# Kernel tuning notes

Measured on AMD Instinct MI355X. Metric: run time of the kernel, lower is better.

Reference implementation:

```python
import jax, jax.numpy as jnp
import numpy as np

SPARSITY = 0.9  # target fraction of zeros (magnitude pruning)
D_IN = 4096
D_OUT = 4096
TOKENS = 4096


def setup_inputs() -> dict:
    key = jax.random.key(0)
    k1, k2 = jax.random.split(key)
    x = jax.random.normal(k1, (TOKENS, D_IN), dtype=jnp.float32)
    weight = jax.random.normal(k2, (D_OUT, D_IN), dtype=jnp.float32) * 0.01
    bias = jnp.zeros((D_OUT,), dtype=jnp.float32)
    return {"x": x, "weight": weight, "bias": bias}


def reference(x, weight, bias):
    # Magnitude pruning: threshold at the SPARSITY quantile of |W|,
    # keep only entries strictly above threshold (matches CSR build),
    # then sparse-dense GEMM y = x @ W_pruned^T + b.
    aw = jnp.abs(weight)
    thr = jnp.quantile(aw, SPARSITY)
    w_pruned = jnp.where(aw > thr, weight, jnp.zeros_like(weight))
    return x @ w_pruned.T + bias
```

## Files before the change

kernel.cpp:

```cpp
#include <hip/hip_runtime.h>
#include <stdint.h>

#define D_IN   4096
#define D_OUT  4096
#define NTOK   4096
#define NW     (D_OUT * D_IN)
#define RANK1  15099493u

typedef unsigned int  uint32;
typedef unsigned short ushort_t;
typedef float  f32x4  __attribute__((ext_vector_type(4)));
typedef __bf16 bf16x8 __attribute__((ext_vector_type(8)));

__device__ __forceinline__ uint32 rne_bf16(float f) {
  uint32 u = __float_as_uint(f);
  return (u + 0x7FFFu + ((u >> 16) & 1u)) >> 16;
}

__device__ __forceinline__ void gload_lds16(const void* g, void* l) {
  __builtin_amdgcn_global_load_lds((__attribute__((address_space(1))) void*)(g),
                                   (__attribute__((address_space(3))) void*)(l), 16, 0, 0);
}

template <int NB>
__device__ __forceinline__ void dsel(const uint32* __restrict__ h, uint32 rank,
                                     uint32* res, uint32* wtot) {
  constexpr int PER = NB >> 8;
  int tid = threadIdx.x;
  int lane = tid & 63, wid = tid >> 6;
  uint32 loc[PER];
  uint32 s = 0;
  int base = tid * PER;
#pragma unroll
  for (int i = 0; i < PER; i++) { loc[i] = h[base + i]; s += loc[i]; }
  uint32 v = s;
  for (int d = 1; d < 64; d <<= 1) { uint32 o = __shfl_up(v, (unsigned)d); if (lane >= d) v += o; }
  if (lane == 63) wtot[wid] = v;
  __syncthreads();
  uint32 woff = 0;
  for (int w = 0; w < wid; w++) woff += wtot[w];
  uint32 incl = v + woff, excl = incl - s;
  if (rank >= excl && rank < incl) {
    uint32 c = excl;
#pragma unroll
    for (int i = 0; i < PER; i++) {
      if (rank < c + loc[i]) { res[0] = (uint32)(base + i); res[1] = rank - c; break; }
      c += loc[i];
    }
  }
  __syncthreads();
}

__global__ void k1_hist1_convx(const uint4* __restrict__ wb, uint32* __restrict__ hist,
                               const float4* __restrict__ x, uint4* __restrict__ xout) {
  __shared__ uint32 lh[4][2048];
  if (blockIdx.x < 2048) {
    for (int i = threadIdx.x; i < 8192; i += 256) ((uint32*)lh)[i] = 0;
    __syncthreads();
    int wid = threadIdx.x >> 6;
    int idx = blockIdx.x * 256 + threadIdx.x;
    for (int i = idx; i < NW / 4; i += 2048 * 256) {
      uint4 v = wb[i];
      atomicAdd(&lh[wid][(v.x & 0x7FFFFFFFu) >> 20], 1u);
      atomicAdd(&lh[wid][(v.y & 0x7FFFFFFFu) >> 20], 1u);
      atomicAdd(&lh[wid][(v.z & 0x7FFFFFFFu) >> 20], 1u);
      atomicAdd(&lh[wid][(v.w & 0x7FFFFFFFu) >> 20], 1u);
    }
    __syncthreads();
    for (int i = threadIdx.x; i < 2048; i += 256) {
      uint32 c = lh[0][i] + lh[1][i] + lh[2][i] + lh[3][i];
      if (c) atomicAdd(&hist[i], c);
    }
  } else {
    int i = (blockIdx.x - 2048) * 256 + threadIdx.x;
    for (; i < NW / 8; i += 1024 * 256) {
      float4 a = x[2 * i], b = x[2 * i + 1];
      uint4 o;
      o.x = rne_bf16(a.x) | (rne_bf16(a.y) << 16);
      o.y = rne_bf16(a.z) | (rne_bf16(a.w) << 16);
      o.z = rne_bf16(b.x) | (rne_bf16(b.y) << 16);
      o.w = rne_bf16(b.z) | (rne_bf16(b.w) << 16);
      xout[i] = o;
    }
  }
}

__global__ void k2_hist2(const uint4* __restrict__ wb, const uint32* __restrict__ hist1,
                         uint32* __restrict__ hist2) {
  __shared__ uint32 lh[1024];
  __shared__ uint32 res1[2], wt[4];
  for (int i = threadIdx.x; i < 1024; i += 256) lh[i] = 0;
  dsel<2048>(hist1, RANK1, res1, wt);
  uint32 pref = res1[0];
  int idx = blockIdx.x * 256 + threadIdx.x;
  for (int i = idx; i < NW / 4; i += 2048 * 256) {
    uint4 v = wb[i];
    uint32 k;
    k = v.x & 0x7FFFFFFFu; if ((k >> 20) == pref) atomicAdd(&lh[(k >> 10) & 1023u], 1u);
    k = v.y & 0x7FFFFFFFu; if ((k >> 20) == pref) atomicAdd(&lh[(k >> 10) & 1023u], 1u);
    k = v.z & 0x7FFFFFFFu; if ((k >> 20) == pref) atomicAdd(&lh[(k >> 10) & 1023u], 1u);
    k = v.w & 0x7FFFFFFFu; if ((k >> 20) == pref) atomicAdd(&lh[(k >> 10) & 1023u], 1u);
  }
  __syncthreads();
  for (int i = threadIdx.x; i < 1024; i += 256) { uint32 c = lh[i]; if (c) atomicAdd(&hist2[i], c); }
}

__global__ void k3_hist3(const uint4* __restrict__ wb, const uint32* __restrict__ hist1,
                         const uint32* __restrict__ hist2, uint32* __restrict__ hist3) {
  __shared__ uint32 lh[1024];
  __shared__ uint32 res1[2], res2[2], wt[4];
  for (int i = threadIdx.x; i < 1024; i += 256) lh[i] = 0;
  dsel<2048>(hist1, RANK1, res1, wt);
  dsel<1024>(hist2, res1[1], res2, wt);
  uint32 pref = (res1[0] << 10) | res2[0];
  int idx = blockIdx.x * 256 + threadIdx.x;
  for (int i = idx; i < NW / 4; i += 2048 * 256) {
    uint4 v = wb[i];
    uint32 k;
    k = v.x & 0x7FFFFFFFu; if ((k >> 10) == pref) atomicAdd(&lh[k & 1023u], 1u);
    k = v.y & 0x7FFFFFFFu; if ((k >> 10) == pref) atomicAdd(&lh[k & 1023u], 1u);
    k = v.z & 0x7FFFFFFFu; if ((k >> 10) == pref) atomicAdd(&lh[k & 1023u], 1u);
    k = v.w & 0x7FFFFFFFu; if ((k >> 10) == pref) atomicAdd(&lh[k & 1023u], 1u);
  }
  __syncthreads();
  for (int i = threadIdx.x; i < 1024; i += 256) { uint32 c = lh[i]; if (c) atomicAdd(&hist3[i], c); }
}

__global__ void k4_convw(const float4* __restrict__ w, const uint32* __restrict__ hist1,
                         const uint32* __restrict__ hist2, const uint32* __restrict__ hist3,
                         uint4* __restrict__ out) {
  __shared__ uint32 res1[2], res2[2], res3[2], wt[4];
  dsel<2048>(hist1, RANK1, res1, wt);
  dsel<1024>(hist2, res1[1], res2, wt);
  dsel<1024>(hist3, res2[1], res3, wt);
  float thr = __uint_as_float((res1[0] << 20) | (res2[0] << 10) | res3[0]);
  int i = blockIdx.x * 256 + threadIdx.x;
  for (; i < NW / 8; i += 2048 * 256) {
    float4 a = w[2 * i], b = w[2 * i + 1];
    float f[8] = {a.x, a.y, a.z, a.w, b.x, b.y, b.z, b.w};
    uint32 h[8];
#pragma unroll
    for (int j = 0; j < 8; j++) h[j] = (fabsf(f[j]) > thr) ? rne_bf16(f[j]) : 0u;
    uint4 o;
    o.x = h[0] | (h[1] << 16);
    o.y = h[2] | (h[3] << 16);
    o.z = h[4] | (h[5] << 16);
    o.w = h[6] | (h[7] << 16);
    out[i] = o;
  }
}

#define TILES 128

__global__ __launch_bounds__(512, 2) void gemm_bt(const ushort_t* __restrict__ A,
                                                  const ushort_t* __restrict__ B,
                                                  const float* __restrict__ bias,
                                                  float* __restrict__ C) {
  extern __shared__ ushort_t lds[];

  int bid = blockIdx.x;
  int swz = (bid & 7) * 32 + (bid >> 3);
  int bm = swz >> 4;
  int bn = swz & 15;

  int tid  = threadIdx.x;
  int lane = tid & 63;
  int wave = tid >> 6;
  int wm = wave >> 2, wn = wave & 3;

  int l15  = lane & 15;
  int csel = (lane >> 4) ^ ((lane >> 1) & 3);

  int idx0 = tid, idx1 = 512 + tid;
  int sr0 = idx0 >> 2, scl0 = (idx0 & 3) ^ ((sr0 >> 1) & 3);
  int sr1 = idx1 >> 2, scl1 = (idx1 & 3) ^ ((sr1 >> 1) & 3);
  int ld0 = idx0 * 8, ld1 = idx1 * 8;
  const ushort_t* pA0 = A + (size_t)(bm * 256 + sr0) * D_IN + scl0 * 8;
  const ushort_t* pA1 = A + (size_t)(bm * 256 + sr1) * D_IN + scl1 * 8;
  const ushort_t* pB0 = B + (size_t)(bn * 256 + sr0) * D_IN + scl0 * 8;
  const ushort_t* pB1 = B + (size_t)(bn * 256 + sr1) * D_IN + scl1 * 8;

  f32x4 acc[8][4];
#pragma unroll
  for (int m = 0; m < 8; m++)
#pragma unroll
    for (int n = 0; n < 4; n++) acc[m][n] = (f32x4){0.f, 0.f, 0.f, 0.f};

  gload_lds16(pA0,      lds + ld0);         gload_lds16(pA1,      lds + ld1);
  gload_lds16(pB0,      lds + 8192 + ld0);  gload_lds16(pB1,      lds + 8192 + ld1);
  gload_lds16(pA0 + 32, lds + 16384 + ld0); gload_lds16(pA1 + 32, lds + 16384 + ld1);
  gload_lds16(pB0 + 32, lds + 24576 + ld0); gload_lds16(pB1 + 32, lds + 24576 + ld1);
  pA0 += 64; pA1 += 64; pB0 += 64; pB1 += 64;
  asm volatile("s_waitcnt vmcnt(4)" ::: "memory");
  asm volatile("s_barrier" ::: "memory");

  int ar = wm * 128 + l15;
  int br = wn * 64 + l15;

  int cur = 0, sd = 2;
  for (int t = 0; t < TILES; t++) {
    ushort_t* sbase = lds + sd * 16384;
    const bf16x8* A8 = (const bf16x8*)(lds + cur * 16384);
    const bf16x8* B8 = A8 + 1024;

    bf16x8 bv0, bv1, bv2, bv3, a0, a1, a2, a3, a4, a5, a6, a7;
    bv0 = B8[(br +  0) * 4 + csel];
    bv1 = B8[(br + 16) * 4 + csel];
    bv2 = B8[(br + 32) * 4 + csel];
    bv3 = B8[(br + 48) * 4 + csel];
    a0  = A8[(ar +  0) * 4 + csel];
    a1  = A8[(ar + 16) * 4 + csel];
    __builtin_amdgcn_sched_barrier(0);
    a2  = A8[(ar + 32) * 4 + csel];
    a3  = A8[(ar + 48) * 4 + csel];
    a4  = A8[(ar + 64) * 4 + csel];
    a5  = A8[(ar + 80) * 4 + csel];
    a6  = A8[(ar + 96) * 4 + csel];
    a7  = A8[(ar + 112) * 4 + csel];
    __builtin_amdgcn_sched_barrier(0);
    gload_lds16(pA0, sbase + ld0);
    gload_lds16(pA1, sbase + ld1);
    gload_lds16(pB0, sbase + 8192 + ld0);
    gload_lds16(pB1, sbase + 8192 + ld1);
    __builtin_amdgcn_sched_barrier(0);

    asm volatile("s_waitcnt lgkmcnt(6)" ::: "memory");
    __builtin_amdgcn_sched_barrier(0);
    __builtin_amdgcn_s_setprio(1);
#pragma unroll
    for (int n = 0; n < 4; n++) {
      bf16x8 bvv = (n == 0) ? bv0 : (n == 1) ? bv1 : (n == 2) ? bv2 : bv3;
      acc[0][n] = __builtin_amdgcn_mfma_f32_16x16x32_bf16(a0, bvv, acc[0][n], 0, 0, 0);
      acc[1][n] = __builtin_amdgcn_mfma_f32_16x16x32_bf16(a1, bvv, acc[1][n], 0, 0, 0);
    }
    __builtin_amdgcn_s_setprio(0);

    asm volatile("s_waitcnt lgkmcnt(4)" ::: "memory");
    __builtin_amdgcn_sched_barrier(0);
    __builtin_amdgcn_s_setprio(1);
#pragma unroll
    for (int n = 0; n < 4; n++) {
      bf16x8 bvv = (n == 0) ? bv0 : (n == 1) ? bv1 : (n == 2) ? bv2 : bv3;
      acc[2][n] = __builtin_amdgcn_mfma_f32_16x16x32_bf16(a2, bvv, acc[2][n], 0, 0, 0);
      acc[3][n] = __builtin_amdgcn_mfma_f32_16x16x32_bf16(a3, bvv, acc[3][n], 0, 0, 0);
    }
    __builtin_amdgcn_s_setprio(0);

    asm volatile("s_waitcnt lgkmcnt(2)" ::: "memory");
    __builtin_amdgcn_sched_barrier(0);
    __builtin_amdgcn_s_setprio(1);
#pragma unroll
    for (int n = 0; n < 4; n++) {
      bf16x8 bvv = (n == 0) ? bv0 : (n == 1) ? bv1 : (n == 2) ? bv2 : bv3;
      acc[4][n] = __builtin_amdgcn_mfma_f32_16x16x32_bf16(a4, bvv, acc[4][n], 0, 0, 0);
      acc[5][n] = __builtin_amdgcn_mfma_f32_16x16x32_bf16(a5, bvv, acc[5][n], 0, 0, 0);
    }
    __builtin_amdgcn_s_setprio(0);

    asm volatile("s_waitcnt vmcnt(4) lgkmcnt(0)" ::: "memory");
    asm volatile("s_barrier" ::: "memory");
    __builtin_amdgcn_sched_barrier(0);
    __builtin_amdgcn_s_setprio(1);
#pragma unroll
    for (int n = 0; n < 4; n++) {
      bf16x8 bvv = (n == 0) ? bv0 : (n == 1) ? bv1 : (n == 2) ? bv2 : bv3;
      acc[6][n] = __builtin_amdgcn_mfma_f32_16x16x32_bf16(a6, bvv, acc[6][n], 0, 0, 0);
      acc[7][n] = __builtin_amdgcn_mfma_f32_16x16x32_bf16(a7, bvv, acc[7][n], 0, 0, 0);
    }
    __builtin_amdgcn_s_setprio(0);

    if (t < TILES - 3) { pA0 += 32; pA1 += 32; pB0 += 32; pB1 += 32; }
    cur = (cur == 2) ? 0 : cur + 1;
    sd  = (sd  == 2) ? 0 : sd + 1;
  }

  int orow0 = bm * 256 + wm * 128 + (lane >> 4) * 4;
  int ocol0 = bn * 256 + wn * 64 + l15;
#pragma unroll
  for (int n = 0; n < 4; n++) {
    float bv2 = bias[ocol0 + n * 16];
#pragma unroll
    for (int m = 0; m < 8; m++) {
#pragma unroll
      for (int r = 0; r < 4; r++) {
        C[(size_t)(orow0 + m * 16 + r) * D_OUT + ocol0 + n * 16] = acc[m][n][r] + bv2;
      }
    }
  }
}

extern "C" void kernel_launch(void* const* d_in, const int* in_sizes, int n_in,
                              void* d_out, int out_size, void* d_ws, size_t ws_size,
                              hipStream_t stream) {
  const float* x = (const float*)d_in[0];
  const float* w = (const float*)d_in[1];
  const float* bias = (const float*)d_in[2];
  float* out = (float*)d_out;

  char* ws = (char*)d_ws;
  uint32* hist1 = (uint32*)ws;
  uint32* hist2 = (uint32*)(ws + 8192);
  uint32* hist3 = (uint32*)(ws + 12288);
  ushort_t* Xb = (ushort_t*)(ws + 65536);
  ushort_t* Wb = (ushort_t*)(ws + 65536 + (size_t)NW * 2);

  hipMemsetAsync(d_ws, 0, 16384, stream);

  k1_hist1_convx<<<3072, 256, 0, stream>>>((const uint4*)w, hist1, (const float4*)x, (uint4*)Xb);
  k2_hist2<<<2048, 256, 0, stream>>>((const uint4*)w, hist1, hist2);
  k3_hist3<<<2048, 256, 0, stream>>>((const uint4*)w, hist1, hist2, hist3);
  k4_convw<<<2048, 256, 0, stream>>>((const float4*)w, hist1, hist2, hist3, (uint4*)Wb);

  gemm_bt<<<256, 512, 98304, stream>>>(Xb, Wb, bias, out);
}
```

Before: 242.1 us.

## Compact threshold candidates and deepen GEMM LDS pipeline to four stages

Replaces the two extra full passes over the weight matrix for the radix-select histogram refinement with a single decide pass. That pass writes bf16 weights for bins clearly above the threshold and compacts same-bin candidates into a list; small kernels then refine the threshold on that list and patch the survivors. Separately, the GEMM moves from a 3-stage to a 4-stage LDS ring and double-buffers register fragments across two unrolled tiles, so LDS reads overlap the MFMAs. Risks: the per-block candidate buffer (3072) and global CAP could overflow and silently drop entries, and using more LDS may reduce occupancy.

Measured after the change: 212.5 us. -12.2%, faster.

```diff
diff --git a/kernel.cpp b/kernel.cpp
--- a/kernel.cpp
+++ b/kernel.cpp
@@ -6,6 +6,7 @@
 #define NTOK   4096
 #define NW     (D_OUT * D_IN)
 #define RANK1  15099493u
+#define CAP    1500000
 
 typedef unsigned int  uint32;
 typedef unsigned short ushort_t;
@@ -85,62 +86,30 @@
   }
 }
 
-__global__ void k2_hist2(const uint4* __restrict__ wb, const uint32* __restrict__ hist1,
-                         uint32* __restrict__ hist2) {
-  __shared__ uint32 lh[1024];
+__global__ void k2_decide(const float4* __restrict__ w, const uint32* __restrict__ hist1,
+                          uint4* __restrict__ out, uint2* __restrict__ cand,
+                          uint32* __restrict__ cnt) {
   __shared__ uint32 res1[2], wt[4];
-  for (int i = threadIdx.x; i < 1024; i += 256) lh[i] = 0;
+  __shared__ uint32 lcnt, lbase;
+  __shared__ uint2 lbuf[3072];
+  if (threadIdx.x == 0) lcnt = 0;
   dsel<2048>(hist1, RANK1, res1, wt);
-  uint32 pref = res1[0];
-  int idx = blockIdx.x * 256 + threadIdx.x;
-  for (int i = idx; i < NW / 4; i += 2048 * 256) {
-    uint4 v = wb[i];
-    uint32 k;
-    k = v.x & 0x7FFFFFFFu; if ((k >> 20) == pref) atomicAdd(&lh[(k >> 10) & 1023u], 1u);
-    k = v.y & 0x7FFFFFFFu; if ((k >> 20) == pref) atomicAdd(&lh[(k >> 10) & 1023u], 1u);
-    k = v.z & 0x7FFFFFFFu; if ((k >> 20) == pref) atomicAdd(&lh[(k >> 10) & 1023u], 1u);
-    k = v.w & 0x7FFFFFFFu; if ((k >> 20) == pref) atomicAdd(&lh[(k >> 10) & 1023u], 1u);
-  }
-  __syncthreads();
-  for (int i = threadIdx.x; i < 1024; i += 256) { uint32 c = lh[i]; if (c) atomicAdd(&hist2[i], c); }
-}
-
-__global__ void k3_hist3(const uint4* __restrict__ wb, const uint32* __restrict__ hist1,
-                         const uint32* __restrict__ hist2, uint32* __restrict__ hist3) {
-  __shared__ uint32 lh[1024];
-  __shared__ uint32 res1[2], res2[2], wt[4];
-  for (int i = threadIdx.x; i < 1024; i += 256) lh[i] = 0;
-  dsel<2048>(hist1, RANK1, res1, wt);
-  dsel<1024>(hist2, res1[1], res2, wt);
-  uint32 pref = (res1[0] << 10) | res2[0];
-  int idx = blockIdx.x * 256 + threadIdx.x;
-  for (int i = idx; i < NW / 4; i += 2048 * 256) {
-    uint4 v = wb[i];
-    uint32 k;
-    k = v.x & 0x7FFFFFFFu; if ((k >> 10) == pref) atomicAdd(&lh[k & 1023u], 1u);
-    k = v.y & 0x7FFFFFFFu; if ((k >> 10) == pref) atomicAdd(&lh[k & 1023u], 1u);
-    k = v.z & 0x7FFFFFFFu; if ((k >> 10) == pref) atomicAdd(&lh[k & 1023u], 1u);
-    k = v.w & 0x7FFFFFFFu; if ((k >> 10) == pref) atomicAdd(&lh[k & 1023u], 1u);
-  }
-  __syncthreads();
-  for (int i = threadIdx.x; i < 1024; i += 256) { uint32 c = lh[i]; if (c) atomicAdd(&hist3[i], c); }
-}
-
-__global__ void k4_convw(const float4* __restrict__ w, const uint32* __restrict__ hist1,
-                         const uint32* __restrict__ hist2, const uint32* __restrict__ hist3,
-                         uint4* __restrict__ out) {
-  __shared__ uint32 res1[2], res2[2], res3[2], wt[4];
-  dsel<2048>(hist1, RANK1, res1, wt);
-  dsel<1024>(hist2, res1[1], res2, wt);
-  dsel<1024>(hist3, res2[1], res3, wt);
-  float thr = __uint_as_float((res1[0] << 20) | (res2[0] << 10) | res3[0]);
+  uint32 bstar = res1[0];
   int i = blockIdx.x * 256 + threadIdx.x;
-  for (; i < NW / 8; i += 2048 * 256) {
+  for (; i < NW / 8; i += 512 * 256) {
     float4 a = w[2 * i], b = w[2 * i + 1];
     float f[8] = {a.x, a.y, a.z, a.w, b.x, b.y, b.z, b.w};
     uint32 h[8];
 #pragma unroll
-    for (int j = 0; j < 8; j++) h[j] = (fabsf(f[j]) > thr) ? rne_bf16(f[j]) : 0u;
+    for (int j = 0; j < 8; j++) {
+      uint32 bits = __float_as_uint(f[j]);
+      uint32 bin = (bits & 0x7FFFFFFFu) >> 20;
+      h[j] = (bin > bstar) ? rne_bf16(f[j]) : 0u;
+      if (bin == bstar) {
+        uint32 p = atomicAdd(&lcnt, 1u);
+        if (p < 3072) lbuf[p] = make_uint2((uint32)(8 * i + j), bits);
+      }
+    }
     uint4 o;
     o.x = h[0] | (h[1] << 16);
     o.y = h[2] | (h[3] << 16);
@@ -148,9 +117,123 @@
     o.w = h[6] | (h[7] << 16);
     out[i] = o;
   }
+  __syncthreads();
+  if (threadIdx.x == 0) lbase = atomicAdd(cnt, lcnt);
+  __syncthreads();
+  for (uint32 p = threadIdx.x; p < lcnt && p < 3072; p += 256) {
+    uint32 g = lbase + p;
+    if (g < CAP) cand[g] = lbuf[p];
+  }
+}
+
+__global__ void s1_hist(const uint2* __restrict__ cand, const uint32* __restrict__ cnt,
+                        uint32* __restrict__ hs1) {
+  __shared__ uint32 lh[1024];
+  for (int i = threadIdx.x; i < 1024; i += 256) lh[i] = 0;
+  __syncthreads();
+  uint32 n = *cnt; if (n > CAP) n = CAP;
+  for (uint32 i = blockIdx.x * 256 + threadIdx.x; i < n; i += gridDim.x * 256) {
+    uint32 mag = cand[i].y & 0x7FFFFFFFu;
+    atomicAdd(&lh[(mag >> 10) & 1023u], 1u);
+  }
+  __syncthreads();
+  for (int i = threadIdx.x; i < 1024; i += 256) if (lh[i]) atomicAdd(&hs1[i], lh[i]);
+}
+
+__global__ void s2_hist(const uint2* __restrict__ cand, const uint32* __restrict__ cnt,
+                        const uint32* __restrict__ hist1, const uint32* __restrict__ hs1,
+                        uint32* __restrict__ hs2) {
+  __shared__ uint32 lh[1024];
+  __shared__ uint32 res1[2], res2[2], wt[4];
+  for (int i = threadIdx.x; i < 1024; i += 256) lh[i] = 0;
+  dsel<2048>(hist1, RANK1, res1, wt);
+  dsel<1024>(hs1, res1[1], res2, wt);
+  uint32 b2 = res2[0];
+  uint32 n = *cnt; if (n > CAP) n = CAP;
+  for (uint32 i = blockIdx.x * 256 + threadIdx.x; i < n; i += gridDim.x * 256) {
+    uint32 mag = cand[i].y & 0x7FFFFFFFu;
+    if (((mag >> 10) & 1023u) == b2) atomicAdd(&lh[mag & 1023u], 1u);
+  }
+  __syncthreads();
+  for (int i = threadIdx.x; i < 1024; i += 256) if (lh[i]) atomicAdd(&hs2[i], lh[i]);
+}
+
+__global__ void k5_fixup(const uint2* __restrict__ cand, const uint32* __restrict__ cnt,
+                         const uint32* __restrict__ hist1, const uint32* __restrict__ hs1,
+                         const uint32* __restrict__ hs2, ushort_t* __restrict__ wb) {
+  __shared__ uint32 res1[2], res2[2], res3[2], wt[4];
+  dsel<2048>(hist1, RANK1, res1, wt);
+  dsel<1024>(hs1, res1[1], res2, wt);
+  dsel<1024>(hs2, res2[1], res3, wt);
+  uint32 thr_mag = (res1[0] << 20) | (res2[0] << 10) | res3[0];
+  uint32 n = *cnt; if (n > CAP) n = CAP;
+  for (uint32 i = blockIdx.x * 256 + threadIdx.x; i < n; i += gridDim.x * 256) {
+    uint2 c = cand[i];
+    uint32 mag = c.y & 0x7FFFFFFFu;
+    if (mag > thr_mag) wb[c.x] = (ushort_t)rne_bf16(__uint_as_float(c.y));
+  }
 }
 
 #define TILES 128
+
+#define MF16(AF, BF, MO)                                                                          \
+  acc[(MO)+0][0] = __builtin_amdgcn_mfma_f32_16x16x32_bf16(AF[0], BF[0], acc[(MO)+0][0], 0,0,0);  \
+  acc[(MO)+0][1] = __builtin_amdgcn_mfma_f32_16x16x32_bf16(AF[0], BF[1], acc[(MO)+0][1], 0,0,0);  \
+  acc[(MO)+0][2] = __builtin_amdgcn_mfma_f32_16x16x32_bf16(AF[0], BF[2], acc[(MO)+0][2], 0,0,0);  \
+  acc[(MO)+0][3] = __builtin_amdgcn_mfma_f32_16x16x32_bf16(AF[0], BF[3], acc[(MO)+0][3], 0,0,0);  \
+  acc[(MO)+1][0] = __builtin_amdgcn_mfma_f32_16x16x32_bf16(AF[1], BF[0], acc[(MO)+1][0], 0,0,0);  \
+  acc[(MO)+1][1] = __builtin_amdgcn_mfma_f32_16x16x32_bf16(AF[1], BF[1], acc[(MO)+1][1], 0,0,0);  \
+  acc[(MO)+1][2] = __builtin_amdgcn_mfma_f32_16x16x32_bf16(AF[1], BF[2], acc[(MO)+1][2], 0,0,0);  \
+  acc[(MO)+1][3] = __builtin_amdgcn_mfma_f32_16x16x32_bf16(AF[1], BF[3], acc[(MO)+1][3], 0,0,0);  \
+  acc[(MO)+2][0] = __builtin_amdgcn_mfma_f32_16x16x32_bf16(AF[2], BF[0], acc[(MO)+2][0], 0,0,0);  \
+  acc[(MO)+2][1] = __builtin_amdgcn_mfma_f32_16x16x32_bf16(AF[2], BF[1], acc[(MO)+2][1], 0,0,0);  \
+  acc[(MO)+2][2] = __builtin_amdgcn_mfma_f32_16x16x32_bf16(AF[2], BF[2], acc[(MO)+2][2], 0,0,0);  \
+  acc[(MO)+2][3] = __builtin_amdgcn_mfma_f32_16x16x32_bf16(AF[2], BF[3], acc[(MO)+2][3], 0,0,0);  \
+  acc[(MO)+3][0] = __builtin_amdgcn_mfma_f32_16x16x32_bf16(AF[3], BF[0], acc[(MO)+3][0], 0,0,0);  \
+  acc[(MO)+3][1] = __builtin_amdgcn_mfma_f32_16x16x32_bf16(AF[3], BF[1], acc[(MO)+3][1], 0,0,0);  \
+  acc[(MO)+3][2] = __builtin_amdgcn_mfma_f32_16x16x32_bf16(AF[3], BF[2], acc[(MO)+3][2], 0,0,0);  \
+  acc[(MO)+3][3] = __builtin_amdgcn_mfma_f32_16x16x32_bf16(AF[3], BF[3], acc[(MO)+3][3], 0,0,0);
+
+#define GBODY(T, S, SN)                                                        \
+  {                                                                            \
+    const bf16x8* A8n = (const bf16x8*)(lds + (((T) + 1) & 3) * 16384);        \
+    const bf16x8* B8n = A8n + 1024;                                            \
+    bv[SN][0]  = B8n[(br +  0) * 4 + csel];                                    \
+    bv[SN][1]  = B8n[(br + 16) * 4 + csel];                                    \
+    bv[SN][2]  = B8n[(br + 32) * 4 + csel];                                    \
+    bv[SN][3]  = B8n[(br + 48) * 4 + csel];                                    \
+    a03[SN][0] = A8n[(ar +  0) * 4 + csel];                                    \
+    a03[SN][1] = A8n[(ar + 16) * 4 + csel];                                    \
+    a03[SN][2] = A8n[(ar + 32) * 4 + csel];                                    \
+    a03[SN][3] = A8n[(ar + 48) * 4 + csel];                                    \
+    __builtin_amdgcn_sched_barrier(0);                                         \
+    ushort_t* sb = lds + (((T) + 3) & 3) * 16384;                              \
+    gload_lds16(pA0, sb + ld0);                                                \
+    gload_lds16(pA1, sb + ld1);                                                \
+    gload_lds16(pB0, sb + 8192 + ld0);                                         \
+    gload_lds16(pB1, sb + 8192 + ld1);                                         \
+    __builtin_amdgcn_sched_barrier(0);                                         \
+    asm volatile("s_waitcnt lgkmcnt(8)" ::: "memory");                         \
+    __builtin_amdgcn_sched_barrier(0);                                         \
+    __builtin_amdgcn_s_setprio(1);                                             \
+    MF16(a47[S], bv[S], 4)                                                     \
+    __builtin_amdgcn_s_setprio(0);                                             \
+    __builtin_amdgcn_sched_barrier(0);                                         \
+    a47[SN][0] = A8n[(ar +  64) * 4 + csel];                                   \
+    a47[SN][1] = A8n[(ar +  80) * 4 + csel];                                   \
+    a47[SN][2] = A8n[(ar +  96) * 4 + csel];                                   \
+    a47[SN][3] = A8n[(ar + 112) * 4 + csel];                                   \
+    __builtin_amdgcn_sched_barrier(0);                                         \
+    asm volatile("s_waitcnt lgkmcnt(4)" ::: "memory");                         \
+    asm volatile("s_waitcnt vmcnt(4)" ::: "memory");                           \
+    asm volatile("s_barrier" ::: "memory");                                    \
+    __builtin_amdgcn_sched_barrier(0);                                         \
+    __builtin_amdgcn_s_setprio(1);                                             \
+    MF16(a03[SN], bv[SN], 0)                                                   \
+    __builtin_amdgcn_s_setprio(0);                                             \
+    __builtin_amdgcn_sched_barrier(0);                                         \
+    if ((T) < TILES - 4) { pA0 += 32; pA1 += 32; pB0 += 32; pB1 += 32; }       \
+  }
 
 __global__ __launch_bounds__(512, 2) void gemm_bt(const ushort_t* __restrict__ A,
                                                   const ushort_t* __restrict__ B,
@@ -190,100 +273,65 @@
   gload_lds16(pB0,      lds + 8192 + ld0);  gload_lds16(pB1,      lds + 8192 + ld1);
   gload_lds16(pA0 + 32, lds + 16384 + ld0); gload_lds16(pA1 + 32, lds + 16384 + ld1);
   gload_lds16(pB0 + 32, lds + 24576 + ld0); gload_lds16(pB1 + 32, lds + 24576 + ld1);
-  pA0 += 64; pA1 += 64; pB0 += 64; pB1 += 64;
+  gload_lds16(pA0 + 64, lds + 32768 + ld0); gload_lds16(pA1 + 64, lds + 32768 + ld1);
+  gload_lds16(pB0 + 64, lds + 40960 + ld0); gload_lds16(pB1 + 64, lds + 40960 + ld1);
+  pA0 += 96; pA1 += 96; pB0 += 96; pB1 += 96;
   asm volatile("s_waitcnt vmcnt(4)" ::: "memory");
   asm volatile("s_barrier" ::: "memory");
 
   int ar = wm * 128 + l15;
   int br = wn * 64 + l15;
 
-  int cur = 0, sd = 2;
-  for (int t = 0; t < TILES; t++) {
-    ushort_t* sbase = lds + sd * 16384;
-    const bf16x8* A8 = (const bf16x8*)(lds + cur * 16384);
+  bf16x8 bv[2][4], a03[2][4], a47[2][4];
+
+  {
+    const bf16x8* A8 = (const bf16x8*)lds;
     const bf16x8* B8 = A8 + 1024;
-
-    bf16x8 bv0, bv1, bv2, bv3, a0, a1, a2, a3, a4, a5, a6, a7;
-    bv0 = B8[(br +  0) * 4 + csel];
-    bv1 = B8[(br + 16) * 4 + csel];
-    bv2 = B8[(br + 32) * 4 + csel];
-    bv3 = B8[(br + 48) * 4 + csel];
-    a0  = A8[(ar +  0) * 4 + csel];
-    a1  = A8[(ar + 16) * 4 + csel];
+    bv[0][0]  = B8[(br +  0) * 4 + csel];
+    bv[0][1]  = B8[(br + 16) * 4 + csel];
+    bv[0][2]  = B8[(br + 32) * 4 + csel];
+    bv[0][3]  = B8[(br + 48) * 4 + csel];
+    a03[0][0] = A8[(ar +  0) * 4 + csel];
+    a03[0][1] = A8[(ar + 16) * 4 + csel];
+    a03[0][2] = A8[(ar + 32) * 4 + csel];
+    a03[0][3] = A8[(ar + 48) * 4 + csel];
     __builtin_amdgcn_sched_barrier(0);
-    a2  = A8[(ar + 32) * 4 + csel];
-    a3  = A8[(ar + 48) * 4 + csel];
-    a4  = A8[(ar + 64) * 4 + csel];
-    a5  = A8[(ar + 80) * 4 + csel];
-    a6  = A8[(ar + 96) * 4 + csel];
-    a7  = A8[(ar + 112) * 4 + csel];
+    a47[0][0] = A8[(ar +  64) * 4 + csel];
+    a47[0][1] = A8[(ar +  80) * 4 + csel];
+    a47[0][2] = A8[(ar +  96) * 4 + csel];
+    a47[0][3] = A8[(ar + 112) * 4 + csel];
     __builtin_amdgcn_sched_barrier(0);
-    gload_lds16(pA0, sbase + ld0);
-    gload_lds16(pA1, sbase + ld1);
-    gload_lds16(pB0, sbase + 8192 + ld0);
-    gload_lds16(pB1, sbase + 8192 + ld1);
-    __builtin_amdgcn_sched_barrier(0);
-
-    asm volatile("s_waitcnt lgkmcnt(6)" ::: "memory");
-    __builtin_amdgcn_sched_barrier(0);
-    __builtin_amdgcn_s_setprio(1);
-#pragma unroll
-    for (int n = 0; n < 4; n++) {
-      bf16x8 bvv = (n == 0) ? bv0 : (n == 1) ? bv1 : (n == 2) ? bv2 : bv3;
-      acc[0][n] = __builtin_amdgcn_mfma_f32_16x16x32_bf16(a0, bvv, acc[0][n], 0, 0, 0);
-      acc[1][n] = __builtin_amdgcn_mfma_f32_16x16x32_bf16(a1, bvv, acc[1][n], 0, 0, 0);
-    }
-    __builtin_amdgcn_s_setprio(0);
-
     asm volatile("s_waitcnt lgkmcnt(4)" ::: "memory");
     __builtin_amdgcn_sched_barrier(0);
     __builtin_amdgcn_s_setprio(1);
-#pragma unroll
-    for (int n = 0; n < 4; n++) {
-      bf16x8 bvv = (n == 0) ? bv0 : (n == 1) ? bv1 : (n == 2) ? bv2 : bv3;
-      acc[2][n] = __builtin_amdgcn_mfma_f32_16x16x32_bf16(a2, bvv, acc[2][n], 0, 0, 0);
-      acc[3][n] = __builtin_amdgcn_mfma_f32_16x16x32_bf16(a3, bvv, acc[3][n], 0, 0, 0);
-    }
+    MF16(a03[0], bv[0], 0)
     __builtin_amdgcn_s_setprio(0);
-
-    asm volatile("s_waitcnt lgkmcnt(2)" ::: "memory");
     __builtin_amdgcn_sched_barrier(0);
-    __builtin_amdgcn_s_setprio(1);
-#pragma unroll
-    for (int n = 0; n < 4; n++) {
-      bf16x8 bvv = (n == 0) ? bv0 : (n == 1) ? bv1 : (n == 2) ? bv2 : bv3;
-      acc[4][n] = __builtin_amdgcn_mfma_f32_16x16x32_bf16(a4, bvv, acc[4][n], 0, 0, 0);
-      acc[5][n] = __builtin_amdgcn_mfma_f32_16x16x32_bf16(a5, bvv, acc[5][n], 0, 0, 0);
-    }
-    __builtin_amdgcn_s_setprio(0);
-
-    asm volatile("s_waitcnt vmcnt(4) lgkmcnt(0)" ::: "memory");
-    asm volatile("s_barrier" ::: "memory");
-    __builtin_amdgcn_sched_barrier(0);
-    __builtin_amdgcn_s_setprio(1);
-#pragma unroll
-    for (int n = 0; n < 4; n++) {
-      bf16x8 bvv = (n == 0) ? bv0 : (n == 1) ? bv1 : (n == 2) ? bv2 : bv3;
-      acc[6][n] = __builtin_amdgcn_mfma_f32_16x16x32_bf16(a6, bvv, acc[6][n], 0, 0, 0);
-      acc[7][n] = __builtin_amdgcn_mfma_f32_16x16x32_bf16(a7, bvv, acc[7][n], 0, 0, 0);
-    }
-    __builtin_amdgcn_s_setprio(0);
-
-    if (t < TILES - 3) { pA0 += 32; pA1 += 32; pB0 += 32; pB1 += 32; }
-    cur = (cur == 2) ? 0 : cur + 1;
-    sd  = (sd  == 2) ? 0 : sd + 1;
-  }
+  }
+
+  for (int tt = 0; tt < 63; tt++) {
+    int t0 = tt * 2;
+    GBODY(t0, 0, 1)
+    GBODY(t0 + 1, 1, 0)
+  }
+  GBODY(126, 0, 1)
+
+  asm volatile("s_waitcnt lgkmcnt(0)" ::: "memory");
+  __builtin_amdgcn_sched_barrier(0);
+  __builtin_amdgcn_s_setprio(1);
+  MF16(a47[1], bv[1], 4)
+  __builtin_amdgcn_s_setprio(0);
 
   int orow0 = bm * 256 + wm * 128 + (lane >> 4) * 4;
   int ocol0 = bn * 256 + wn * 64 + l15;
 #pragma unroll
   for (int n = 0; n < 4; n++) {
-    float bv2 = bias[ocol0 + n * 16];
+    float bb = bias[ocol0 + n * 16];
 #pragma unroll
     for (int m = 0; m < 8; m++) {
 #pragma unroll
       for (int r = 0; r < 4; r++) {
-        C[(size_t)(orow0 + m * 16 + r) * D_OUT + ocol0 + n * 16] = acc[m][n][r] + bv2;
+        C[(size_t)(orow0 + m * 16 + r) * D_OUT + ocol0 + n * 16] = acc[m][n][r] + bb;
       }
     }
   }
@@ -299,17 +347,20 @@
 
   char* ws = (char*)d_ws;
   uint32* hist1 = (uint32*)ws;
-  uint32* hist2 = (uint32*)(ws + 8192);
-  uint32* hist3 = (uint32*)(ws + 12288);
-  ushort_t* Xb = (ushort_t*)(ws + 65536);
-  ushort_t* Wb = (ushort_t*)(ws + 65536 + (size_t)NW * 2);
-
-  hipMemsetAsync(d_ws, 0, 16384, stream);
+  uint32* hs1   = (uint32*)(ws + 8192);
+  uint32* hs2   = (uint32*)(ws + 12288);
+  uint32* cnt   = (uint32*)(ws + 16384);
+  ushort_t* Xb  = (ushort_t*)(ws + 65536);
+  ushort_t* Wb  = (ushort_t*)(ws + 65536 + (size_t)NW * 2);
+  uint2*   cand = (uint2*)(ws + 65536 + (size_t)NW * 4);
+
+  hipMemsetAsync(d_ws, 0, 16448, stream);
 
   k1_hist1_convx<<<3072, 256, 0, stream>>>((const uint4*)w, hist1, (const float4*)x, (uint4*)Xb);
-  k2_hist2<<<2048, 256, 0, stream>>>((const uint4*)w, hist1, hist2);
-  k3_hist3<<<2048, 256, 0, stream>>>((const uint4*)w, hist1, hist2, hist3);
-  k4_convw<<<2048, 256, 0, stream>>>((const float4*)w, hist1, hist2, hist3, (uint4*)Wb);
-
-  gemm_bt<<<256, 512, 98304, stream>>>(Xb, Wb, bias, out);
-}
+  k2_decide<<<512, 256, 0, stream>>>((const float4*)w, hist1, (uint4*)Wb, cand, cnt);
+  s1_hist<<<128, 256, 0, stream>>>(cand, cnt, hs1);
+  s2_hist<<<128, 256, 0, stream>>>(cand, cnt, hist1, hs1, hs2);
+  k5_fixup<<<256, 256, 0, stream>>>(cand, cnt, hist1, hs1, hs2, Wb);
+
+  gemm_bt<<<256, 512, 131072, stream>>>(Xb, Wb, bias, out);
+}
```
